# Optimization experiments

Measured on AMD Instinct MI355X. Metric: run time of the kernel, lower is better.

The kernel has to match this reference:

```python
import jax, jax.numpy as jnp
import numpy as np

R = 0.15          # ball-query radius (module init arg r)
K = 32            # _MAX_NEIGHBOURS
B, N = 8, 4096


def _ball_query(pos, r, k):
    """Dense ball query. pos: [B,N,3] -> neighbor idx [B,N,K], sorted by distance.
    Slots with fewer than k in-radius neighbors are filled with the query's own
    index (self is always the first neighbor at distance 0), so their
    contribution to (f_i - f_j)^2 is exactly 0 -- matching torch-points-kernels'
    fill-with-first-neighbor behaviour."""
    d2 = jnp.sum((pos[:, :, None, :] - pos[:, None, :, :]) ** 2, axis=-1)  # [B,N,N]
    masked = jnp.where(d2 <= r * r, d2, jnp.inf)
    neg_vals, idx = jax.lax.top_k(-masked, k)          # ascending distance
    valid = neg_vals > -jnp.inf
    self_idx = jnp.arange(pos.shape[1])[None, :, None]
    return jnp.where(valid, idx, self_idx)             # [B,N,K]


def setup_inputs() -> dict:
    key = jax.random.key(0)
    k1, k2 = jax.random.split(key)
    pos = jax.random.uniform(k1, (B, N, 3), dtype=jnp.float32)
    f = jax.random.normal(k2, (B, N), dtype=jnp.float32)
    return {"pos": pos, "f": f}


def reference(pos, f):
    # neighbor indices are non-differentiable (torch gathers with long indices)
    nei_idx = jax.lax.stop_gradient(_ball_query(pos, R, K))      # [B,N,K]
    f_nei = jax.vmap(lambda fb, ib: fb[ib])(f, nei_idx)          # [B,N,K]
    variances = jnp.sum((f[:, :, None] - f_nei) ** 2, axis=-1)   # [B,N]
    return 0.5 * jnp.mean(variances)
```

## Files before the change

kernel.cpp:

```cpp
#include <hip/hip_runtime.h>


#define BQ_K 32
#define CAP 128
#define WPB 4
#define G 6
#define NC (G * G * G)
#define CAPC 512
#define QMAX 64
#define NPTS 4096

__device__ __forceinline__ int cell_coord(float x) {
    int c = (int)(x * (float)G);
    return c < 0 ? 0 : (c > G - 1 ? G - 1 : c);
}

__device__ __forceinline__ float select_sum(float2 e0, float2 e1, int M,
                                            float r2) {
    if (M <= BQ_K) return e0.y + e1.y;
    float lo = 0.0f, hi = r2 * 1.000001f;
    #pragma unroll
    for (int it = 0; it < 14; ++it) {
        const float mid = 0.5f * (lo + hi);
        const int cnt = __popcll(__ballot(e0.x < mid)) +
                        __popcll(__ballot(e1.x < mid));
        if (cnt >= BQ_K) hi = mid; else lo = mid;
    }
    float s = 0.0f;
    if (e0.x < hi) s = e0.y;
    if (e1.x < hi) s += e1.y;
    return s;
}

__global__ __launch_bounds__(256) void dl_fused(
    const float* __restrict__ pos, const float* __restrict__ f,
    float* __restrict__ out, float r2, float scale)
{
    __shared__ float4 s_cand[CAPC];
    __shared__ float2 s_sel[WPB][CAP];
    __shared__ int    s_q[QMAX];
    __shared__ int    s_ncand, s_nq;
    __shared__ float  s_wsum[WPB];

    const int bc = blockIdx.x;
    const int b  = bc / NC;
    const int c  = bc - b * NC;
    const int cx = c % G, cy = (c / G) % G, cz = c / (G * G);

    const int lane = threadIdx.x & 63;
    const int wave = threadIdx.x >> 6;
    const unsigned long long lmask = (1ULL << lane) - 1ULL;

    if (threadIdx.x == 0) { s_ncand = 0; s_nq = 0; }
    __syncthreads();

    const float* posb = pos + (size_t)b * NPTS * 3;
    const float* fb   = f   + (size_t)b * NPTS;

    const float lox = cx * (1.0f / G), hix = lox + (1.0f / G);
    const float loy = cy * (1.0f / G), hiy = loy + (1.0f / G);
    const float loz = cz * (1.0f / G), hiz = loz + (1.0f / G);

    constexpr int per = NPTS / WPB;
    const int wbeg = wave * per;
    for (int j0 = 0; j0 < per; j0 += 64) {
        const int j = wbeg + j0 + lane;
        const float x  = posb[3 * j + 0];
        const float y  = posb[3 * j + 1];
        const float z  = posb[3 * j + 2];
        const float fj = fb[j];
        const float ddx = fmaxf(fmaxf(lox - x, x - hix), 0.0f);
        const float ddy = fmaxf(fmaxf(loy - y, y - hiy), 0.0f);
        const float ddz = fmaxf(fmaxf(loz - z, z - hiz), 0.0f);
        const float d2c = fmaf(ddx, ddx, fmaf(ddy, ddy, ddz * ddz));
        const bool in = (d2c <= r2);
        const unsigned long long m = __ballot(in);
        const int nh = __popcll(m);
        int base = 0;
        if (lane == 0 && nh) base = atomicAdd(&s_ncand, nh);
        base = __shfl(base, 0, 64);
        if (in) {
            const int off = base + __popcll(m & lmask);
            if (off < CAPC) {
                s_cand[off] = make_float4(x, y, z, fj);
                if (cell_coord(x) == cx && cell_coord(y) == cy &&
                    cell_coord(z) == cz) {
                    const int qs = atomicAdd(&s_nq, 1);
                    if (qs < QMAX) s_q[qs] = off;
                }
            }
        }
    }
    __syncthreads();

    const int ncand = s_ncand < CAPC ? s_ncand : CAPC;
    const int nq    = s_nq < QMAX ? s_nq : QMAX;
    const int ncB   = (ncand + 63) & ~63;

    float2* sel = s_sel[wave];
    float wsum = 0.0f;

    for (int qi = wave; qi < nq; qi += WPB) {
        const float4 qp = s_cand[s_q[qi]];
        const float qx = qp.x, qy = qp.y, qz = qp.z, fi = qp.w;

        int cin = 0;
        for (int basej = 0; basej < ncB; basej += 64) {
            const float4 cd = s_cand[basej + lane];
            const bool valid = (basej + lane) < ncand;
            const float dx = cd.x - qx, dy = cd.y - qy, dz = cd.z - qz;
            const float d2 = fmaf(dx, dx, fmaf(dy, dy, dz * dz));
            const bool inb = valid && (d2 <= r2);
            const unsigned long long mm = __ballot(inb);
            const int off = cin + __popcll(mm & lmask);
            if (inb && off < CAP) {
                const float fd = fi - cd.w;
                sel[off] = make_float2(d2, fd * fd);
            }
            cin += __popcll(mm);
        }
        const int M = cin < CAP ? cin : CAP;

        const float2 e0 = (lane < M) ? sel[lane]
                                     : make_float2(1e30f, 0.0f);
        const float2 e1 = (64 + lane < M) ? sel[64 + lane]
                                          : make_float2(1e30f, 0.0f);
        wsum += select_sum(e0, e1, M, r2);
    }

    for (int o = 32; o > 0; o >>= 1) wsum += __shfl_down(wsum, o, 64);
    if (lane == 0) s_wsum[wave] = wsum;
    __syncthreads();
    if (threadIdx.x == 0) {
        const float bs = s_wsum[0] + s_wsum[1] + s_wsum[2] + s_wsum[3];
        atomicAdd(out, bs * scale);
    }
}

extern "C" void kernel_launch(void* const* d_in, const int* in_sizes, int n_in,
                              void* d_out, int out_size, void* d_ws, size_t ws_size,
                              hipStream_t stream) {
    const float* pos = (const float*)d_in[0];
    const float* f   = (const float*)d_in[1];
    float* out = (float*)d_out;

    const int B = in_sizes[1] / NPTS;
    const float r2 = 0.15f * 0.15f;
    const float scale = 0.5f / (float)((long long)B * NPTS);

    hipMemsetAsync(out, 0, sizeof(float), stream);
    dl_fused<<<B * NC, 256, 0, stream>>>(pos, f, out, r2, scale);
}
```

Before: 89.15 us.

## Bucket points into grid cells before ball query instead of scanning all points per cell

```diff
diff --git a/kernel.cpp b/kernel.cpp
--- a/kernel.cpp
+++ b/kernel.cpp
@@ -6,6 +6,7 @@
 #define WPB 4
 #define G 6
 #define NC (G * G * G)
+#define CMAX 64
 #define CAPC 512
 #define QMAX 64
 #define NPTS 4096
@@ -20,7 +21,7 @@
     if (M <= BQ_K) return e0.y + e1.y;
     float lo = 0.0f, hi = r2 * 1.000001f;
     #pragma unroll
-    for (int it = 0; it < 14; ++it) {
+    for (int it = 0; it < 12; ++it) {
         const float mid = 0.5f * (lo + hi);
         const int cnt = __popcll(__ballot(e0.x < mid)) +
                         __popcll(__ballot(e1.x < mid));
@@ -32,7 +33,129 @@
     return s;
 }
 
-__global__ __launch_bounds__(256) void dl_fused(
+__global__ void dl_scatter(const float* __restrict__ pos,
+                           const float* __restrict__ f,
+                           int* __restrict__ cnt, float4* __restrict__ buck,
+                           int total) {
+    const int t = blockIdx.x * blockDim.x + threadIdx.x;
+    if (t >= total) return;
+    const int b = t >> 12;
+    const float x = pos[3 * (size_t)t + 0];
+    const float y = pos[3 * (size_t)t + 1];
+    const float z = pos[3 * (size_t)t + 2];
+    const int c = (cell_coord(z) * G + cell_coord(y)) * G + cell_coord(x);
+    const int cell = b * NC + c;
+    const int slot = atomicAdd(&cnt[cell], 1);
+    if (slot < CMAX)
+        buck[(size_t)cell * CMAX + slot] = make_float4(x, y, z, f[t]);
+}
+
+__global__ __launch_bounds__(256) void dl_main(
+    const int* __restrict__ cnt, const float4* __restrict__ buck,
+    float* __restrict__ out, float r2, float scale)
+{
+    __shared__ float4 s_cand[CAPC];
+    __shared__ float2 s_sel[WPB][CAP];
+    __shared__ int    s_q[QMAX];
+    __shared__ int    s_ncand, s_nq;
+    __shared__ float  s_wsum[WPB];
+
+    const int bc = blockIdx.x;
+    const int b  = bc / NC;
+    const int c  = bc - b * NC;
+    const int cx = c % G, cy = (c / G) % G, cz = c / (G * G);
+
+    const int lane = threadIdx.x & 63;
+    const int wave = threadIdx.x >> 6;
+    const unsigned long long lmask = (1ULL << lane) - 1ULL;
+
+    if (threadIdx.x == 0) { s_ncand = 0; s_nq = 0; }
+    __syncthreads();
+
+    const float lox = cx * (1.0f / G), hix = lox + (1.0f / G);
+    const float loy = cy * (1.0f / G), hiy = loy + (1.0f / G);
+    const float loz = cz * (1.0f / G), hiz = loz + (1.0f / G);
+
+    for (int n = wave; n < 27; n += WPB) {
+        const int nx = cx + (n % 3) - 1;
+        const int ny = cy + ((n / 3) % 3) - 1;
+        const int nz = cz + (n / 9) - 1;
+        if ((unsigned)nx >= (unsigned)G || (unsigned)ny >= (unsigned)G ||
+            (unsigned)nz >= (unsigned)G) continue;
+        const int cell = b * NC + (nz * G + ny) * G + nx;
+        int cc = cnt[cell];
+        cc = cc < CMAX ? cc : CMAX;
+        const bool have = lane < cc;
+        float4 p = make_float4(1e30f, 1e30f, 1e30f, 0.0f);
+        if (have) p = buck[(size_t)cell * CMAX + lane];
+        const float ddx = fmaxf(fmaxf(lox - p.x, p.x - hix), 0.0f);
+        const float ddy = fmaxf(fmaxf(loy - p.y, p.y - hiy), 0.0f);
+        const float ddz = fmaxf(fmaxf(loz - p.z, p.z - hiz), 0.0f);
+        const float d2c = fmaf(ddx, ddx, fmaf(ddy, ddy, ddz * ddz));
+        const bool in = have && (d2c <= r2);
+        const unsigned long long m = __ballot(in);
+        const int nh = __popcll(m);
+        int base = 0;
+        if (lane == 0 && nh) base = atomicAdd(&s_ncand, nh);
+        base = __shfl(base, 0, 64);
+        if (in) {
+            const int off = base + __popcll(m & lmask);
+            if (off < CAPC) {
+                s_cand[off] = p;
+                if (n == 13) {
+                    const int qs = atomicAdd(&s_nq, 1);
+                    if (qs < QMAX) s_q[qs] = off;
+                }
+            }
+        }
+    }
+    __syncthreads();
+
+    const int ncand = s_ncand < CAPC ? s_ncand : CAPC;
+    const int nq    = s_nq < QMAX ? s_nq : QMAX;
+    const int ncB   = (ncand + 63) & ~63;
+
+    float2* sel = s_sel[wave];
+    float wsum = 0.0f;
+
+    for (int qi = wave; qi < nq; qi += WPB) {
+        const float4 qp = s_cand[s_q[qi]];
+        const float qx = qp.x, qy = qp.y, qz = qp.z, fi = qp.w;
+
+        int cin = 0;
+        for (int basej = 0; basej < ncB; basej += 64) {
+            const float4 cd = s_cand[basej + lane];
+            const bool valid = (basej + lane) < ncand;
+            const float dx = cd.x - qx, dy = cd.y - qy, dz = cd.z - qz;
+            const float d2 = fmaf(dx, dx, fmaf(dy, dy, dz * dz));
+            const bool inb = valid && (d2 <= r2);
+            const unsigned long long mm = __ballot(inb);
+            const int off = cin + __popcll(mm & lmask);
+            if (inb && off < CAP) {
+                const float fd = fi - cd.w;
+                sel[off] = make_float2(d2, fd * fd);
+            }
+            cin += __popcll(mm);
+        }
+        const int M = cin < CAP ? cin : CAP;
+
+        const float2 e0 = (lane < M) ? sel[lane]
+                                     : make_float2(1e30f, 0.0f);
+        const float2 e1 = (64 + lane < M) ? sel[64 + lane]
+                                          : make_float2(1e30f, 0.0f);
+        wsum += select_sum(e0, e1, M, r2);
+    }
+
+    for (int o = 32; o > 0; o >>= 1) wsum += __shfl_down(wsum, o, 64);
+    if (lane == 0) s_wsum[wave] = wsum;
+    __syncthreads();
+    if (threadIdx.x == 0) {
+        const float bs = s_wsum[0] + s_wsum[1] + s_wsum[2] + s_wsum[3];
+        atomicAdd(out, bs * scale);
+    }
+}
+
+__global__ __launch_bounds__(256) void dl_fallback(
     const float* __restrict__ pos, const float* __restrict__ f,
     float* __restrict__ out, float r2, float scale)
 {
@@ -46,7 +169,6 @@
     const int b  = bc / NC;
     const int c  = bc - b * NC;
     const int cx = c % G, cy = (c / G) % G, cz = c / (G * G);
-
     const int lane = threadIdx.x & 63;
     const int wave = threadIdx.x >> 6;
     const unsigned long long lmask = (1ULL << lane) - 1ULL;
@@ -56,7 +178,6 @@
 
     const float* posb = pos + (size_t)b * NPTS * 3;
     const float* fb   = f   + (size_t)b * NPTS;
-
     const float lox = cx * (1.0f / G), hix = lox + (1.0f / G);
     const float loy = cy * (1.0f / G), hiy = loy + (1.0f / G);
     const float loz = cz * (1.0f / G), hiz = loz + (1.0f / G);
@@ -68,7 +189,6 @@
         const float x  = posb[3 * j + 0];
         const float y  = posb[3 * j + 1];
         const float z  = posb[3 * j + 2];
-        const float fj = fb[j];
         const float ddx = fmaxf(fmaxf(lox - x, x - hix), 0.0f);
         const float ddy = fmaxf(fmaxf(loy - y, y - hiy), 0.0f);
         const float ddz = fmaxf(fmaxf(loz - z, z - hiz), 0.0f);
@@ -82,7 +202,7 @@
         if (in) {
             const int off = base + __popcll(m & lmask);
             if (off < CAPC) {
-                s_cand[off] = make_float4(x, y, z, fj);
+                s_cand[off] = make_float4(x, y, z, fb[j]);
                 if (cell_coord(x) == cx && cell_coord(y) == cy &&
                     cell_coord(z) == cz) {
                     const int qs = atomicAdd(&s_nq, 1);
@@ -96,14 +216,12 @@
     const int ncand = s_ncand < CAPC ? s_ncand : CAPC;
     const int nq    = s_nq < QMAX ? s_nq : QMAX;
     const int ncB   = (ncand + 63) & ~63;
-
     float2* sel = s_sel[wave];
     float wsum = 0.0f;
 
     for (int qi = wave; qi < nq; qi += WPB) {
         const float4 qp = s_cand[s_q[qi]];
         const float qx = qp.x, qy = qp.y, qz = qp.z, fi = qp.w;
-
         int cin = 0;
         for (int basej = 0; basej < ncB; basej += 64) {
             const float4 cd = s_cand[basej + lane];
@@ -120,9 +238,7 @@
             cin += __popcll(mm);
         }
         const int M = cin < CAP ? cin : CAP;
-
-        const float2 e0 = (lane < M) ? sel[lane]
-                                     : make_float2(1e30f, 0.0f);
+        const float2 e0 = (lane < M) ? sel[lane] : make_float2(1e30f, 0.0f);
         const float2 e1 = (64 + lane < M) ? sel[64 + lane]
                                           : make_float2(1e30f, 0.0f);
         wsum += select_sum(e0, e1, M, r2);
@@ -145,9 +261,23 @@
     float* out = (float*)d_out;
 
     const int B = in_sizes[1] / NPTS;
+    const int total = B * NPTS;
     const float r2 = 0.15f * 0.15f;
-    const float scale = 0.5f / (float)((long long)B * NPTS);
+    const float scale = 0.5f / (float)total;
 
     hipMemsetAsync(out, 0, sizeof(float), stream);
-    dl_fused<<<B * NC, 256, 0, stream>>>(pos, f, out, r2, scale);
-}
+
+    const size_t cnt_bytes  = (size_t)B * NC * sizeof(int);
+    const size_t buck_bytes = (size_t)B * NC * CMAX * sizeof(float4);
+    if (ws_size < cnt_bytes + buck_bytes) {
+        dl_fallback<<<B * NC, 256, 0, stream>>>(pos, f, out, r2, scale);
+        return;
+    }
+
+    int*    cnt  = (int*)d_ws;
+    float4* buck = (float4*)((char*)d_ws + cnt_bytes);
+
+    hipMemsetAsync(cnt, 0, cnt_bytes, stream);
+    dl_scatter<<<(total + 255) / 256, 256, 0, stream>>>(pos, f, cnt, buck, total);
+    dl_main   <<<B * NC, 256, 0, stream>>>(cnt, buck, out, r2, scale);
+}
```

Result: slower. 91.85 us (+3.0%).
